# Optimization experiments

Measured on AMD Instinct MI355X. Metric: run time of the kernel, lower is better.

## Reference

```python
import math
import jax, jax.numpy as jnp
import numpy as np

B, S, HID, NH = 2, 2048, 2048, 16
HD = HID // NH          # 128
QKD = HD // 2           # 64
BASE = 10000.0
LAYER_ID = 1
LAMBDA_INIT = 0.8 - 0.6 * math.exp(-0.3 * LAYER_ID)
EPS = 1e-6


def _rope_tables():
    i = np.arange(0, HD, 2, dtype=np.float32)
    theta = BASE ** (-i / HD)                      # [HD/2]
    pos = np.arange(S, dtype=np.float32)
    m_theta = np.outer(pos, theta)                 # [S, HD/2]
    cos = np.repeat(np.cos(m_theta), 2, axis=1)    # [S, HD]
    sin = np.repeat(np.sin(m_theta), 2, axis=1)
    return jnp.asarray(cos), jnp.asarray(sin)


def setup_inputs() -> dict:
    key = jax.random.key(0)
    ks = jax.random.split(key, 12)
    wstd = 0.02
    cos_emb, sin_emb = _rope_tables()
    return {
        "q": jax.random.normal(ks[0], (B, S, HID), jnp.float32),
        "k": jax.random.normal(ks[1], (B, S, HID), jnp.float32),
        "v": jax.random.normal(ks[2], (B, S, HID), jnp.float32),
        "Wq": jax.random.normal(ks[3], (HID, HID), jnp.float32) * wstd,
        "Wk": jax.random.normal(ks[4], (HID, HID), jnp.float32) * wstd,
        "Wv": jax.random.normal(ks[5], (HID, HID), jnp.float32) * wstd,
        "Wo": jax.random.normal(ks[6], (HID, HID), jnp.float32) * wstd,
        "lambda_q1": jax.random.normal(ks[7], (HD,), jnp.float32) * 0.1,
        "lambda_k1": jax.random.normal(ks[8], (HD,), jnp.float32) * 0.1,
        "lambda_q2": jax.random.normal(ks[9], (HD,), jnp.float32) * 0.1,
        "lambda_k2": jax.random.normal(ks[10], (HD,), jnp.float32) * 0.1,
        "gnorm_w": jnp.ones((HD,), jnp.float32),
        "cos_emb": cos_emb,
        "sin_emb": sin_emb,
        "mask": jnp.triu(jnp.ones((S, S), bool), 1),  # causal: True = masked
    }


def _apply_rope(x, cos_emb, sin_emb):
    # x: [B, 2, H, S, QKD]; tables sliced to [:S, :QKD] as in the torch code
    cos = cos_emb[:S, :QKD][None, None, None]
    sin = sin_emb[:S, :QKD][None, None, None]
    inv = jnp.stack((-x[..., 1::2], x[..., 0::2]), axis=-1).reshape(x.shape)
    return x * cos + inv * sin


def reference(q, k, v, Wq, Wk, Wv, Wo, lambda_q1, lambda_k1, lambda_q2,
              lambda_k2, gnorm_w, cos_emb, sin_emb, mask):
    lin = lambda x, W: jnp.einsum('bsi,oi->bso', x, W)  # torch Linear: x @ W.T
    qh = lin(q, Wq).reshape(B, S, NH, 2, QKD).transpose(0, 3, 2, 1, 4)  # [B,2,H,S,QKD]
    kh = lin(k, Wk).reshape(B, S, NH, 2, QKD).transpose(0, 3, 2, 1, 4)
    vh = lin(v, Wv).reshape(B, S, NH, HD).transpose(0, 2, 1, 3)          # [B,H,S,HD]
    qh = _apply_rope(qh, cos_emb, sin_emb)
    kh = _apply_rope(kh, cos_emb, sin_emb)

    scores = jnp.einsum('bghsd,bghtd->bghst', qh, kh) / math.sqrt(QKD)   # [B,2,H,S,S]
    scores = jnp.where(mask, jnp.finfo(jnp.float32).min, scores)

    lam1 = jnp.exp(jnp.sum(lambda_q1 * lambda_k1))
    lam2 = jnp.exp(jnp.sum(lambda_q2 * lambda_k2))
    lam = lam1 - lam2 + LAMBDA_INIT

    attn = jax.nn.softmax(scores[:, 0], axis=-1) - lam * jax.nn.softmax(scores[:, 1], axis=-1)
    out = jnp.einsum('bhst,bhtd->bhsd', attn, vh)                        # [B,H,S,HD]

    rms = out * jax.lax.rsqrt(jnp.mean(out * out, axis=-1, keepdims=True) + EPS) * gnorm_w
    out = (1.0 - LAMBDA_INIT) * rms
    out = out.transpose(0, 2, 1, 3).reshape(B, S, HID)
    return lin(out, Wo)
```

## Files before the change

### kernel.cpp

```cpp
#include <hip/hip_runtime.h>
#include <math.h>

#define BDIM 2
#define SDIM 2048
#define HIDD 2048
#define NHH 16
#define HDD 128
#define QKDD 64
#define MTOT (BDIM*SDIM)

constexpr float LAMBDA_INIT_F = 0.3555090675909693f;
constexpr float EPS_F = 1e-6f;
constexpr float SCALE_F = 0.125f;

typedef float f32x4 __attribute__((ext_vector_type(4)));
typedef short bf16x8 __attribute__((ext_vector_type(8)));
typedef short bf16x4 __attribute__((ext_vector_type(4)));

#define MFMA16(a, b, c) __builtin_amdgcn_mfma_f32_16x16x32_bf16((a), (b), (c), 0, 0, 0)

__device__ __forceinline__ short f2bf(float f) {
    unsigned u = __float_as_uint(f);
    u += 0x7FFFu + ((u >> 16) & 1u);
    return (short)(u >> 16);
}
__device__ __forceinline__ unsigned pk2(float a, float b) {
    return (unsigned)(unsigned short)f2bf(a) | ((unsigned)(unsigned short)f2bf(b) << 16);
}

__device__ __forceinline__ void gload_lds16(const void* g, void* l) {
    __builtin_amdgcn_global_load_lds(
        (const __attribute__((address_space(1))) void*)g,
        (__attribute__((address_space(3))) void*)l, 16, 0, 0);
}

__global__ void lambda_kernel(const float* __restrict__ lq1, const float* __restrict__ lk1,
                              const float* __restrict__ lq2, const float* __restrict__ lk2,
                              float* __restrict__ lam_out) {
    int l = threadIdx.x;
    float d1 = lq1[l] * lk1[l] + lq1[l + 64] * lk1[l + 64];
    float d2 = lq2[l] * lk2[l] + lq2[l + 64] * lk2[l + 64];
#pragma unroll
    for (int o = 32; o > 0; o >>= 1) {
        d1 += __shfl_down(d1, o);
        d2 += __shfl_down(d2, o);
    }
    if (l == 0) lam_out[0] = expf(d1) - expf(d2) + LAMBDA_INIT_F;
}

__global__ __launch_bounds__(256) void f32_to_bf16(const float* __restrict__ in,
                                                   short* __restrict__ out, int n) {
    int i = (blockIdx.x * 256 + threadIdx.x) * 8;
    if (i >= n) return;
    float4 a = *(const float4*)&in[i];
    float4 b = *(const float4*)&in[i + 4];
    uint4 o;
    o.x = pk2(a.x, a.y); o.y = pk2(a.z, a.w);
    o.z = pk2(b.x, b.y); o.w = pk2(b.z, b.w);
    *(uint4*)&out[i] = o;
}

template<int MODE>
__global__ __launch_bounds__(256) void gemm_bf16(const short* __restrict__ Ab,
                                                 const short* __restrict__ Bb,
                                                 void* __restrict__ Cv,
                                                 const float* __restrict__ cosE,
                                                 const float* __restrict__ sinE,
                                                 int M, int N, int K) {
    __shared__ short As[128 * 32];
    __shared__ short Bs[128 * 32];
    const int tid = threadIdx.x;
    const int w = tid >> 6, lane = tid & 63;
    const int lq = lane & 15, lg = lane >> 4;
    const int wr = w >> 1, wc = w & 1;
    const int bm = blockIdx.y * 128;
    const int bn = blockIdx.x * 128;

    const size_t aoff = (size_t)(bm + w * 16 + (lane >> 2)) * K + (lane & 3) * 8;
    const size_t boff = (size_t)(bn + w * 16 + (lane >> 2)) * K + (lane & 3) * 8;
    const size_t rowskip = (size_t)64 * K;

    f32x4 acc[4][4] = {};

    for (int k0 = 0; k0 < K; k0 += 32) {
        __syncthreads();
        gload_lds16(Ab + aoff + k0,           &As[w * 512]);
        gload_lds16(Ab + aoff + rowskip + k0, &As[(w + 4) * 512]);
        gload_lds16(Bb + boff + k0,           &Bs[w * 512]);
        gload_lds16(Bb + boff + rowskip + k0, &Bs[(w + 4) * 512]);
        __syncthreads();

        bf16x8 a[4], b[4];
#pragma unroll
        for (int m = 0; m < 4; ++m)
            a[m] = *(const bf16x8*)&As[(wr * 64 + m * 16 + lq) * 32 + lg * 8];
#pragma unroll
        for (int n = 0; n < 4; ++n)
            b[n] = *(const bf16x8*)&Bs[(wc * 64 + n * 16 + lq) * 32 + lg * 8];
#pragma unroll
        for (int m = 0; m < 4; ++m)
#pragma unroll
            for (int n = 0; n < 4; ++n)
                acc[m][n] = MFMA16(a[m], b[n], acc[m][n]);
    }

    if constexpr (MODE == 0) {
        float* C = (float*)Cv;
#pragma unroll
        for (int m = 0; m < 4; ++m)
#pragma unroll
            for (int n = 0; n < 4; ++n) {
                const int row0 = bm + wr * 64 + m * 16 + lg * 4;
                const int col  = bn + wc * 64 + n * 16 + lq;
#pragma unroll
                for (int r = 0; r < 4; ++r)
                    C[(size_t)(row0 + r) * N + col] = acc[m][n][r];
            }
    } else {
        short* Cb = (short*)Cv;
#pragma unroll
        for (int m = 0; m < 4; ++m)
#pragma unroll
            for (int n = 0; n < 4; ++n) {
                const int row0 = bm + wr * 64 + m * 16 + lg * 4;
                const int col  = bn + wc * 64 + n * 16 + lq;
#pragma unroll
                for (int r = 0; r < 4; ++r) {
                    float vv = acc[m][n][r];
                    if constexpr (MODE == 2) {
                        const int s  = (row0 + r) & (SDIM - 1);
                        const int c6 = col & 63;
                        const float cv = cosE[s * HDD + c6];
                        const float sv = sinE[s * HDD + c6];
                        const float p = __shfl_xor(vv, 1);
                        vv = (col & 1) ? vv * cv + p * sv : vv * cv - p * sv;
                    }
                    Cb[(size_t)(row0 + r) * N + col] = f2bf(vv);
                }
            }
    }
}

#define KVB 64

__device__ __forceinline__ bf16x8 pack_pa(const float p0[4], const float p1[4]) {
    union { unsigned u[4]; bf16x8 v; } r;
    r.u[0] = pk2(p0[0], p0[1]);
    r.u[1] = pk2(p0[2], p0[3]);
    r.u[2] = pk2(p1[0], p1[1]);
    r.u[3] = pk2(p1[2], p1[3]);
    return r.v;
}

__device__ __forceinline__ void softmax_step(
        f32x4 sc[4], float& M, float& L, f32x4 O[8], bf16x8 pa[2],
        int t0, int qg, int lg, bool domask) {
#pragma unroll
    for (int sub = 0; sub < 4; ++sub)
#pragma unroll
        for (int r = 0; r < 4; ++r) {
            float s = sc[sub][r] * SCALE_F;
            if (domask) {
                int key = t0 + sub * 16 + lg * 4 + r;
                s = (key <= qg) ? s : -1e30f;
            }
            sc[sub][r] = s;
        }
    float mx = -1e30f;
#pragma unroll
    for (int sub = 0; sub < 4; ++sub) {
        float a01 = fmaxf(sc[sub][0], sc[sub][1]);
        float a23 = fmaxf(sc[sub][2], sc[sub][3]);
        mx = fmaxf(mx, fmaxf(a01, a23));
    }
    mx = fmaxf(mx, __shfl_xor(mx, 16));
    mx = fmaxf(mx, __shfl_xor(mx, 32));
    if (__ballot(mx > M + 8.f)) {
        const float Mn = fmaxf(M, mx);
        const float a = __expf(M - Mn);
        M = Mn;
        L *= a;
        float ar[4];
#pragma unroll
        for (int r = 0; r < 4; ++r) ar[r] = __shfl(a, lg * 4 + r);
#pragma unroll
        for (int d = 0; d < 8; ++d) {
            O[d][0] *= ar[0]; O[d][1] *= ar[1]; O[d][2] *= ar[2]; O[d][3] *= ar[3];
        }
    }
    float p[4][4];
    float ps = 0.f;
#pragma unroll
    for (int sub = 0; sub < 4; ++sub) {
#pragma unroll
        for (int r = 0; r < 4; ++r) p[sub][r] = __expf(sc[sub][r] - M);
        ps += (p[sub][0] + p[sub][1]) + (p[sub][2] + p[sub][3]);
    }
    ps += __shfl_xor(ps, 16);
    ps += __shfl_xor(ps, 32);
    L += ps;
    pa[0] = pack_pa(p[0], p[1]);
    pa[1] = pack_pa(p[2], p[3]);
}

__global__ __launch_bounds__(256, 2) void flash_mfma(
        const short* __restrict__ Qb, const short* __restrict__ Kb,
        const short* __restrict__ Vb, const float* __restrict__ gnw,
        const float* __restrict__ lam_p, short* __restrict__ Hob) {
    __shared__ short Ksh[KVB * 128];
    __shared__ short VT[HDD * 72];

    const int tid = threadIdx.x;
    const int w  = tid >> 6;
    const int l  = tid & 63;
    const int lq = l & 15;
    const int lg = l >> 4;

    const int blk = blockIdx.x;
    const int bh  = blk & 31;
    const int bx  = 31 - (blk >> 5);
    const int b = bh >> 4, h = bh & 15;
    const int s0 = bx * 64;
    const float lam = lam_p[0];

    const int qg = s0 + w * 16 + lq;
    const short* qrow = Qb + ((size_t)(b * SDIM + qg)) * HIDD + h * HDD;
    bf16x8 qf[2][2];
#pragma unroll
    for (int br = 0; br < 2; ++br)
#pragma unroll
        for (int ks = 0; ks < 2; ++ks)
            qf[br][ks] = *(const bf16x8*)(qrow + br * 64 + ks * 32 + lg * 8);

    int kkey[4], kcol[4];
#pragma unroll
    for (int i = 0; i < 4; ++i) {
        kkey[i] = w * 16 + i * 4 + lg;
        kcol[i] = (lq * 8) ^ ((kkey[i] & 7) << 3);
    }
    const int kp = tid & 31, dq = tid >> 5;

    const short* Kbase = Kb + ((size_t)(b * SDIM)) * HIDD + h * HDD;
    const short* Vbase = Vb + ((size_t)(b * SDIM)) * HIDD + h * HDD;

    float M1 = -1e30f, M2 = -1e30f, L1 = 0.f, L2 = 0.f;
    f32x4 O1[8] = {}; f32x4 O2[8] = {};

    const int ntmax = bx + 1;
    const int qmin = s0 + w * 16;
    const int ntw = (qmin >> 6) + 1;

    for (int t = 0; t < ntmax; ++t) {
        const size_t trow = (size_t)t * KVB * HIDD;
        __syncthreads();
#pragma unroll
        for (int i = 0; i < 4; ++i)
            gload_lds16(Kbase + trow + (size_t)kkey[i] * HIDD + kcol[i],
                        &Ksh[w * 2048 + i * 512]);
        {
            const short* v0 = Vbase + trow + (size_t)(2 * kp) * HIDD + dq * 16;
            const short* v1 = v0 + HIDD;
            bf16x8 v00 = *(const bf16x8*)v0;
            bf16x8 v01 = *(const bf16x8*)(v0 + 8);
            bf16x8 v10 = *(const bf16x8*)v1;
            bf16x8 v11 = *(const bf16x8*)(v1 + 8);
#pragma unroll
            for (int j = 0; j < 8; ++j) {
                unsigned ua = (unsigned)(unsigned short)v00[j] |
                              ((unsigned)(unsigned short)v10[j] << 16);
                *(unsigned*)&VT[(dq * 16 + j) * 72 + 2 * kp] = ua;
                unsigned ub = (unsigned)(unsigned short)v01[j] |
                              ((unsigned)(unsigned short)v11[j] << 16);
                *(unsigned*)&VT[(dq * 16 + 8 + j) * 72 + 2 * kp] = ub;
            }
        }
        __syncthreads();
        if (t >= ntw) continue;

        f32x4 sc1[4] = {}; f32x4 sc2[4] = {};
        const int rsw = (lq & 7) << 3;
#pragma unroll
        for (int sub = 0; sub < 4; ++sub) {
            const int rbase = (sub * 16 + lq) * 128;
            bf16x8 k00 = *(const bf16x8*)&Ksh[rbase + ((lg * 8) ^ rsw)];
            bf16x8 k01 = *(const bf16x8*)&Ksh[rbase + ((32 + lg * 8) ^ rsw)];
            bf16x8 k10 = *(const bf16x8*)&Ksh[rbase + ((64 + lg * 8) ^ rsw)];
            bf16x8 k11 = *(const bf16x8*)&Ksh[rbase + ((96 + lg * 8) ^ rsw)];
            sc1[sub] = MFMA16(k00, qf[0][0], sc1[sub]);
            sc1[sub] = MFMA16(k01, qf[0][1], sc1[sub]);
            sc2[sub] = MFMA16(k10, qf[1][0], sc2[sub]);
            sc2[sub] = MFMA16(k11, qf[1][1], sc2[sub]);
        }
        const int t0 = t * KVB;
        const bool domask = (t0 + KVB - 1 > qmin);
        bf16x8 pa1[2], pa2[2];
        softmax_step(sc1, M1, L1, O1, pa1, t0, qg, lg, domask);
        softmax_step(sc2, M2, L2, O2, pa2, t0, qg, lg, domask);

#pragma unroll
        for (int d0 = 0; d0 < 8; ++d0) {
            const short* vrow = &VT[(d0 * 16 + lq) * 72];
            bf16x4 a0 = *(const bf16x4*)&vrow[lg * 4];
            bf16x4 a1 = *(const bf16x4*)&vrow[16 + lg * 4];
            bf16x4 b0 = *(const bf16x4*)&vrow[32 + lg * 4];
            bf16x4 b1 = *(const bf16x4*)&vrow[48 + lg * 4];
            bf16x8 vb0 = __builtin_shufflevector(a0, a1, 0, 1, 2, 3, 4, 5, 6, 7);
            bf16x8 vb1 = __builtin_shufflevector(b0, b1, 0, 1, 2, 3, 4, 5, 6, 7);
            O1[d0] = MFMA16(pa1[0], vb0, O1[d0]);
            O1[d0] = MFMA16(pa1[1], vb1, O1[d0]);
            O2[d0] = MFMA16(pa2[0], vb0, O2[d0]);
            O2[d0] = MFMA16(pa2[1], vb1, O2[d0]);
        }
    }

    const float inv1 = 1.f / L1;
    const float inv2 = lam / L2;
    float i1[4], i2[4];
#pragma unroll
    for (int r = 0; r < 4; ++r) {
        i1[r] = __shfl(inv1, lg * 4 + r);
        i2[r] = __shfl(inv2, lg * 4 + r);
    }
    float gn[8];
#pragma unroll
    for (int d = 0; d < 8; ++d) gn[d] = gnw[d * 16 + lq];
    float od[8][4];
    float ss[4] = {0.f, 0.f, 0.f, 0.f};
#pragma unroll
    for (int d = 0; d < 8; ++d)
#pragma unroll
        for (int r = 0; r < 4; ++r) {
            float o = O1[d][r] * i1[r] - O2[d][r] * i2[r];
            od[d][r] = o;
            ss[r] += o * o;
        }
#pragma unroll
    for (int r = 0; r < 4; ++r) {
        ss[r] += __shfl_xor(ss[r], 1);
        ss[r] += __shfl_xor(ss[r], 2);
        ss[r] += __shfl_xor(ss[r], 4);
        ss[r] += __shfl_xor(ss[r], 8);
    }
#pragma unroll
    for (int r = 0; r < 4; ++r) {
        const float scal = rsqrtf(ss[r] * (1.0f / HDD) + EPS_F) * (1.0f - LAMBDA_INIT_F);
        const size_t orow = ((size_t)(b * SDIM + s0 + w * 16 + lg * 4 + r)) * HIDD + h * HDD;
#pragma unroll
        for (int d = 0; d < 8; ++d)
            Hob[orow + d * 16 + lq] = f2bf(od[d][r] * scal * gn[d]);
    }
}

extern "C" void kernel_launch(void* const* d_in, const int* in_sizes, int n_in,
                              void* d_out, int out_size, void* d_ws, size_t ws_size,
                              hipStream_t stream) {
    const float* q   = (const float*)d_in[0];
    const float* k   = (const float*)d_in[1];
    const float* v   = (const float*)d_in[2];
    const float* Wq  = (const float*)d_in[3];
    const float* Wk  = (const float*)d_in[4];
    const float* Wv  = (const float*)d_in[5];
    const float* Wo  = (const float*)d_in[6];
    const float* lq1 = (const float*)d_in[7];
    const float* lk1 = (const float*)d_in[8];
    const float* lq2 = (const float*)d_in[9];
    const float* lk2 = (const float*)d_in[10];
    const float* gnw = (const float*)d_in[11];
    const float* cosE = (const float*)d_in[12];
    const float* sinE = (const float*)d_in[13];
    float* out = (float*)d_out;

    const size_t TEN = (size_t)BDIM * SDIM * HIDD;
    const int   WN  = HIDD * HIDD;

    short* wsS = (short*)d_ws;
    short* Qb   = wsS;
    short* Kb   = wsS + TEN;
    short* Vb   = wsS + 2 * TEN;
    short* xb   = wsS + 3 * TEN;
    short* wb   = wsS + 4 * TEN;
    float* lamp = (float*)(wsS + 4 * TEN + WN);

    lambda_kernel<<<1, 64, 0, stream>>>(lq1, lk1, lq2, lk2, lamp);

    const int cgX = (int)(TEN / 8 / 256);
    const int cgW = WN / 8 / 256;
    dim3 gg(HIDD / 128, MTOT / 128);

    f32_to_bf16<<<cgX, 256, 0, stream>>>(q, xb, (int)TEN);
    f32_to_bf16<<<cgW, 256, 0, stream>>>(Wq, wb, WN);
    gemm_bf16<2><<<gg, 256, 0, stream>>>(xb, wb, Qb, cosE, sinE, MTOT, HIDD, HIDD);

    f32_to_bf16<<<cgX, 256, 0, stream>>>(k, xb, (int)TEN);
    f32_to_bf16<<<cgW, 256, 0, stream>>>(Wk, wb, WN);
    gemm_bf16<2><<<gg, 256, 0, stream>>>(xb, wb, Kb, cosE, sinE, MTOT, HIDD, HIDD);

    f32_to_bf16<<<cgX, 256, 0, stream>>>(v, xb, (int)TEN);
    f32_to_bf16<<<cgW, 256, 0, stream>>>(Wv, wb, WN);
    gemm_bf16<1><<<gg, 256, 0, stream>>>(xb, wb, Vb, nullptr, nullptr, MTOT, HIDD, HIDD);

    flash_mfma<<<(SDIM / 64) * BDIM * NHH, 256, 0, stream>>>(Qb, Kb, Vb, gnw, lamp, xb);

    f32_to_bf16<<<cgW, 256, 0, stream>>>(Wo, wb, WN);
    gemm_bf16<0><<<gg, 256, 0, stream>>>(xb, wb, out, nullptr, nullptr, MTOT, HIDD, HIDD);
}
```

Measured before the change: 374.6 us.

## Batch conversions and QKV GEMMs, deepen K tile with swizzled LDS

Merges the separate f32-to-bf16 conversion launches into two batched kernels and runs the three Q/K/V projections as one grid with a z dimension. The GEMM main loop now loads a 64-wide K slice per iteration into an XOR-swizzled LDS layout, which halves the number of barrier pairs and is meant to avoid bank conflicts. This needs more workspace for the staged bf16 inputs and weights, and doubles the LDS used per block.

Measured after the change: 330.6 us. -11.7%, faster.

```diff
diff --git a/kernel.cpp b/kernel.cpp
--- a/kernel.cpp
+++ b/kernel.cpp
@@ -48,97 +48,152 @@
     if (l == 0) lam_out[0] = expf(d1) - expf(d2) + LAMBDA_INIT_F;
 }
 
-__global__ __launch_bounds__(256) void f32_to_bf16(const float* __restrict__ in,
-                                                   short* __restrict__ out, int n) {
+__global__ __launch_bounds__(256) void conv_x(const float* __restrict__ s0,
+                                              const float* __restrict__ s1,
+                                              const float* __restrict__ s2,
+                                              short* __restrict__ dst, int n) {
+    const float* src = (blockIdx.y == 0) ? s0 : (blockIdx.y == 1) ? s1 : s2;
+    short* out = dst + (size_t)blockIdx.y * n;
     int i = (blockIdx.x * 256 + threadIdx.x) * 8;
     if (i >= n) return;
-    float4 a = *(const float4*)&in[i];
-    float4 b = *(const float4*)&in[i + 4];
+    float4 a = *(const float4*)&src[i];
+    float4 b = *(const float4*)&src[i + 4];
     uint4 o;
     o.x = pk2(a.x, a.y); o.y = pk2(a.z, a.w);
     o.z = pk2(b.x, b.y); o.w = pk2(b.z, b.w);
     *(uint4*)&out[i] = o;
 }
-
-template<int MODE>
-__global__ __launch_bounds__(256) void gemm_bf16(const short* __restrict__ Ab,
-                                                 const short* __restrict__ Bb,
-                                                 void* __restrict__ Cv,
-                                                 const float* __restrict__ cosE,
-                                                 const float* __restrict__ sinE,
-                                                 int M, int N, int K) {
-    __shared__ short As[128 * 32];
-    __shared__ short Bs[128 * 32];
+__global__ __launch_bounds__(256) void conv_w(const float* __restrict__ s0,
+                                              const float* __restrict__ s1,
+                                              const float* __restrict__ s2,
+                                              const float* __restrict__ s3,
+                                              short* __restrict__ dst, int n) {
+    const float* src = (blockIdx.y == 0) ? s0 : (blockIdx.y == 1) ? s1
+                     : (blockIdx.y == 2) ? s2 : s3;
+    short* out = dst + (size_t)blockIdx.y * n;
+    int i = (blockIdx.x * 256 + threadIdx.x) * 8;
+    if (i >= n) return;
+    float4 a = *(const float4*)&src[i];
+    float4 b = *(const float4*)&src[i + 4];
+    uint4 o;
+    o.x = pk2(a.x, a.y); o.y = pk2(a.z, a.w);
+    o.z = pk2(b.x, b.y); o.w = pk2(b.z, b.w);
+    *(uint4*)&out[i] = o;
+}
+
+#define GK 2048
+
+__device__ __forceinline__ void gemm_mainloop(
+        const short* __restrict__ X, const short* __restrict__ W,
+        short* As, short* Bs, f32x4 acc[4][4],
+        int bm, int bn, int w, int l, int lq, int lg, int wr, int wc) {
+    const int scol = (((l & 7) ^ (l >> 3)) << 3);
+    const int rsw  = (lq & 7) << 3;
+    const short* aS[4]; const short* bS[4];
+    short* aD[4]; short* bD[4];
+#pragma unroll
+    for (int i = 0; i < 4; ++i) {
+        const int c = w * 4 + i;
+        aS[i] = X + (size_t)(bm + c * 8 + (l >> 3)) * GK + scol;
+        bS[i] = W + (size_t)(bn + c * 8 + (l >> 3)) * GK + scol;
+        aD[i] = As + c * 512;
+        bD[i] = Bs + c * 512;
+    }
+    for (int k0 = 0; k0 < GK; k0 += 64) {
+        __syncthreads();
+#pragma unroll
+        for (int i = 0; i < 4; ++i) {
+            gload_lds16(aS[i] + k0, aD[i]);
+            gload_lds16(bS[i] + k0, bD[i]);
+        }
+        __syncthreads();
+#pragma unroll
+        for (int kk = 0; kk < 2; ++kk) {
+            bf16x8 a[4], b[4];
+#pragma unroll
+            for (int m = 0; m < 4; ++m)
+                a[m] = *(const bf16x8*)&As[(wr * 64 + m * 16 + lq) * 64 + ((kk * 32 + lg * 8) ^ rsw)];
+#pragma unroll
+            for (int n = 0; n < 4; ++n)
+                b[n] = *(const bf16x8*)&Bs[(wc * 64 + n * 16 + lq) * 64 + ((kk * 32 + lg * 8) ^ rsw)];
+#pragma unroll
+            for (int m = 0; m < 4; ++m)
+#pragma unroll
+                for (int n = 0; n < 4; ++n)
+                    acc[m][n] = MFMA16(a[m], b[n], acc[m][n]);
+        }
+    }
+}
+
+__global__ __launch_bounds__(256) void qkv_gemm(
+        const short* __restrict__ Xq, const short* __restrict__ Xk, const short* __restrict__ Xv,
+        const short* __restrict__ Wb, short* __restrict__ Qb, short* __restrict__ Kb,
+        short* __restrict__ Vb, const float* __restrict__ cosE, const float* __restrict__ sinE) {
+    __shared__ short As[128 * 64];
+    __shared__ short Bs[128 * 64];
     const int tid = threadIdx.x;
-    const int w = tid >> 6, lane = tid & 63;
-    const int lq = lane & 15, lg = lane >> 4;
+    const int w = tid >> 6, l = tid & 63;
+    const int lq = l & 15, lg = l >> 4;
     const int wr = w >> 1, wc = w & 1;
     const int bm = blockIdx.y * 128;
     const int bn = blockIdx.x * 128;
-
-    const size_t aoff = (size_t)(bm + w * 16 + (lane >> 2)) * K + (lane & 3) * 8;
-    const size_t boff = (size_t)(bn + w * 16 + (lane >> 2)) * K + (lane & 3) * 8;
-    const size_t rowskip = (size_t)64 * K;
+    const int z  = blockIdx.z;
+
+    const short* X = (z == 0) ? Xq : (z == 1) ? Xk : Xv;
+    const short* W = Wb + (size_t)z * HIDD * HIDD;
+    short* Cb      = (z == 0) ? Qb : (z == 1) ? Kb : Vb;
 
     f32x4 acc[4][4] = {};
-
-    for (int k0 = 0; k0 < K; k0 += 32) {
-        __syncthreads();
-        gload_lds16(Ab + aoff + k0,           &As[w * 512]);
-        gload_lds16(Ab + aoff + rowskip + k0, &As[(w + 4) * 512]);
-        gload_lds16(Bb + boff + k0,           &Bs[w * 512]);
-        gload_lds16(Bb + boff + rowskip + k0, &Bs[(w + 4) * 512]);
-        __syncthreads();
-
-        bf16x8 a[4], b[4];
-#pragma unroll
-        for (int m = 0; m < 4; ++m)
-            a[m] = *(const bf16x8*)&As[(wr * 64 + m * 16 + lq) * 32 + lg * 8];
-#pragma unroll
-        for (int n = 0; n < 4; ++n)
-            b[n] = *(const bf16x8*)&Bs[(wc * 64 + n * 16 + lq) * 32 + lg * 8];
-#pragma unroll
-        for (int m = 0; m < 4; ++m)
-#pragma unroll
-            for (int n = 0; n < 4; ++n)
-                acc[m][n] = MFMA16(a[m], b[n], acc[m][n]);
-    }
-
-    if constexpr (MODE == 0) {
-        float* C = (float*)Cv;
-#pragma unroll
-        for (int m = 0; m < 4; ++m)
-#pragma unroll
-            for (int n = 0; n < 4; ++n) {
-                const int row0 = bm + wr * 64 + m * 16 + lg * 4;
-                const int col  = bn + wc * 64 + n * 16 + lq;
-#pragma unroll
-                for (int r = 0; r < 4; ++r)
-                    C[(size_t)(row0 + r) * N + col] = acc[m][n][r];
+    gemm_mainloop(X, W, As, Bs, acc, bm, bn, w, l, lq, lg, wr, wc);
+
+    const bool dorope = (z < 2);
+#pragma unroll
+    for (int m = 0; m < 4; ++m)
+#pragma unroll
+        for (int n = 0; n < 4; ++n) {
+            const int row0 = bm + wr * 64 + m * 16 + lg * 4;
+            const int col  = bn + wc * 64 + n * 16 + lq;
+#pragma unroll
+            for (int r = 0; r < 4; ++r) {
+                float vv = acc[m][n][r];
+                if (dorope) {
+                    const int s  = (row0 + r) & (SDIM - 1);
+                    const int c6 = col & 63;
+                    const float cv = cosE[s * HDD + c6];
+                    const float sv = sinE[s * HDD + c6];
+                    const float p = __shfl_xor(vv, 1);
+                    vv = (col & 1) ? vv * cv + p * sv : vv * cv - p * sv;
+                }
+                Cb[(size_t)(row0 + r) * HIDD + col] = f2bf(vv);
             }
-    } else {
-        short* Cb = (short*)Cv;
-#pragma unroll
-        for (int m = 0; m < 4; ++m)
-#pragma unroll
-            for (int n = 0; n < 4; ++n) {
-                const int row0 = bm + wr * 64 + m * 16 + lg * 4;
-                const int col  = bn + wc * 64 + n * 16 + lq;
-#pragma unroll
-                for (int r = 0; r < 4; ++r) {
-                    float vv = acc[m][n][r];
-                    if constexpr (MODE == 2) {
-                        const int s  = (row0 + r) & (SDIM - 1);
-                        const int c6 = col & 63;
-                        const float cv = cosE[s * HDD + c6];
-                        const float sv = sinE[s * HDD + c6];
-                        const float p = __shfl_xor(vv, 1);
-                        vv = (col & 1) ? vv * cv + p * sv : vv * cv - p * sv;
-                    }
-                    Cb[(size_t)(row0 + r) * N + col] = f2bf(vv);
-                }
-            }
-    }
+        }
+}
+
+__global__ __launch_bounds__(256) void o_gemm(const short* __restrict__ Ab,
+                                              const short* __restrict__ Bb,
+                                              float* __restrict__ C) {
+    __shared__ short As[128 * 64];
+    __shared__ short Bs[128 * 64];
+    const int tid = threadIdx.x;
+    const int w = tid >> 6, l = tid & 63;
+    const int lq = l & 15, lg = l >> 4;
+    const int wr = w >> 1, wc = w & 1;
+    const int bm = blockIdx.y * 128;
+    const int bn = blockIdx.x * 128;
+
+    f32x4 acc[4][4] = {};
+    gemm_mainloop(Ab, Bb, As, Bs, acc, bm, bn, w, l, lq, lg, wr, wc);
+
+#pragma unroll
+    for (int m = 0; m < 4; ++m)
+#pragma unroll
+        for (int n = 0; n < 4; ++n) {
+            const int row0 = bm + wr * 64 + m * 16 + lg * 4;
+            const int col  = bn + wc * 64 + n * 16 + lq;
+#pragma unroll
+            for (int r = 0; r < 4; ++r)
+                C[(size_t)(row0 + r) * HIDD + col] = acc[m][n][r];
+        }
 }
 
 #define KVB 64
@@ -377,30 +432,24 @@
     short* Qb   = wsS;
     short* Kb   = wsS + TEN;
     short* Vb   = wsS + 2 * TEN;
-    short* xb   = wsS + 3 * TEN;
-    short* wb   = wsS + 4 * TEN;
-    float* lamp = (float*)(wsS + 4 * TEN + WN);
+    short* xqkv = wsS + 3 * TEN;
+    short* wb4  = wsS + 6 * TEN;
+    float* lamp = (float*)(wsS + 6 * TEN + (size_t)4 * WN);
+    short* Hob  = xqkv;
 
     lambda_kernel<<<1, 64, 0, stream>>>(lq1, lk1, lq2, lk2, lamp);
 
-    const int cgX = (int)(TEN / 8 / 256);
-    const int cgW = WN / 8 / 256;
-    dim3 gg(HIDD / 128, MTOT / 128);
-
-    f32_to_bf16<<<cgX, 256, 0, stream>>>(q, xb, (int)TEN);
-    f32_to_bf16<<<cgW, 256, 0, stream>>>(Wq, wb, WN);
-    gemm_bf16<2><<<gg, 256, 0, stream>>>(xb, wb, Qb, cosE, sinE, MTOT, HIDD, HIDD);
-
-    f32_to_bf16<<<cgX, 256, 0, stream>>>(k, xb, (int)TEN);
-    f32_to_bf16<<<cgW, 256, 0, stream>>>(Wk, wb, WN);
-    gemm_bf16<2><<<gg, 256, 0, stream>>>(xb, wb, Kb, cosE, sinE, MTOT, HIDD, HIDD);
-
-    f32_to_bf16<<<cgX, 256, 0, stream>>>(v, xb, (int)TEN);
-    f32_to_bf16<<<cgW, 256, 0, stream>>>(Wv, wb, WN);
-    gemm_bf16<1><<<gg, 256, 0, stream>>>(xb, wb, Vb, nullptr, nullptr, MTOT, HIDD, HIDD);
-
-    flash_mfma<<<(SDIM / 64) * BDIM * NHH, 256, 0, stream>>>(Qb, Kb, Vb, gnw, lamp, xb);
-
-    f32_to_bf16<<<cgW, 256, 0, stream>>>(Wo, wb, WN);
-    gemm_bf16<0><<<gg, 256, 0, stream>>>(xb, wb, out, nullptr, nullptr, MTOT, HIDD, HIDD);
-}
+    dim3 gx((int)(TEN / 8 / 256), 3);
+    conv_x<<<gx, 256, 0, stream>>>(q, k, v, xqkv, (int)TEN);
+    dim3 gw(WN / 8 / 256, 4);
+    conv_w<<<gw, 256, 0, stream>>>(Wq, Wk, Wv, Wo, wb4, WN);
+
+    dim3 gq(HIDD / 128, MTOT / 128, 3);
+    qkv_gemm<<<gq, 256, 0, stream>>>(xqkv, xqkv + TEN, xqkv + 2 * TEN, wb4,
+                                     Qb, Kb, Vb, cosE, sinE);
+
+    flash_mfma<<<(SDIM / 64) * BDIM * NHH, 256, 0, stream>>>(Qb, Kb, Vb, gnw, lamp, Hob);
+
+    dim3 go(HIDD / 128, MTOT / 128);
+    o_gemm<<<go, 256, 0, stream>>>(Hob, wb4 + (size_t)3 * WN, out);
+}
```
